# Performance work log

Hardware: AMD Instinct MI355X
Metric: run time of the kernel (lower is better)

## Reference

```python
import jax, jax.numpy as jnp
import numpy as np

N_NODES = 100000
N_EDGES = 3200000  # avg degree 32
D_IN = 128
D_OUT = 64
BN_EPS = 0.001


def setup_inputs() -> dict:
    key = jax.random.key(0)
    k1, k2, k3, k4, k5 = jax.random.split(key, 5)
    x = jax.random.normal(k1, (N_NODES, D_IN), dtype=jnp.float32)
    W = jax.random.normal(k2, (D_IN, D_OUT), dtype=jnp.float32) * 0.05
    edge_val = jax.random.uniform(k3, (N_EDGES,), dtype=jnp.float32)
    edge_src = jax.random.randint(k4, (N_EDGES,), 0, N_NODES, dtype=jnp.int32)
    edge_dst = jax.random.randint(k5, (N_EDGES,), 0, N_NODES, dtype=jnp.int32)
    return {"x": x, "W": W, "edge_val": edge_val,
            "edge_src": edge_src, "edge_dst": edge_dst}


def reference(x, W, edge_val, edge_src, edge_dst):
    # pre_sup = X @ W  (dense feature transform; dropout rate is 0 -> identity)
    pre_sup = x @ W  # [N, D_OUT]
    # support = A @ pre_sup, A given in COO form: A[dst, src] = edge_val
    msgs = edge_val[:, None] * pre_sup[edge_src]          # [E, D_OUT]
    out = jax.ops.segment_sum(msgs, edge_dst, num_segments=N_NODES)  # [N, D_OUT]
    # tf.nn.moments over all-but-last axis + batch_norm (no scale/offset, eps=1e-3)
    mean = jnp.mean(out, axis=0)
    var = jnp.var(out, axis=0)
    out = (out - mean) * jax.lax.rsqrt(var + BN_EPS)
    return jax.nn.relu(out)
```

## Files before the change

### kernel.cpp

```cpp
#include <hip/hip_runtime.h>
#include <stdint.h>

#define D_IN  128
#define D_OUT 64
#define BN_EPS 1e-3f

#define BIN_SHIFT 6
#define BIN_NODES 64
#define BIN_CAP   2560
#define CHUNK     8192
#define MAX_BINS  1600

typedef __attribute__((ext_vector_type(8))) short bf16x8;
typedef __attribute__((ext_vector_type(4))) float f32x4;

__device__ __forceinline__ ushort f32_to_bf16_rne(float f) {
  uint u = __float_as_uint(f);
  u += 0x7FFFu + ((u >> 16) & 1u);
  return (ushort)(u >> 16);
}
__device__ __forceinline__ float bf16_to_f32(ushort h) {
  return __uint_as_float((uint)h << 16);
}

__global__ __launch_bounds__(256) void gemm_mfma_kernel(
    const float* __restrict__ x, const float* __restrict__ W,
    ushort* __restrict__ pre16, int n_nodes, int n_tiles) {
  __shared__ ushort Wb[D_IN * D_OUT];
  const int t = threadIdx.x;
  for (int i = t; i < D_IN * D_OUT; i += 256) Wb[i] = f32_to_bf16_rne(W[i]);
  __syncthreads();

  const int lane = t & 63;
  const int wave = t >> 6;
  const int m = lane & 15;
  const int quad = lane >> 4;

  bf16x8 bfrag[4][4];
#pragma unroll
  for (int nt = 0; nt < 4; ++nt)
#pragma unroll
    for (int s = 0; s < 4; ++s)
#pragma unroll
      for (int j = 0; j < 8; ++j)
        bfrag[nt][s][j] =
            (short)Wb[(32 * s + quad * 8 + j) * D_OUT + nt * 16 + m];

  for (int tile = blockIdx.x; tile < n_tiles; tile += gridDim.x) {
    const int rbase = tile * 64 + wave * 16;
    const int row = rbase + m;
    const size_t rl = (size_t)min(row, n_nodes - 1);
    f32x4 acc0 = {0.f, 0.f, 0.f, 0.f}, acc1 = {0.f, 0.f, 0.f, 0.f};
    f32x4 acc2 = {0.f, 0.f, 0.f, 0.f}, acc3 = {0.f, 0.f, 0.f, 0.f};
#pragma unroll
    for (int s = 0; s < 4; ++s) {
      const float4 xa = *(const float4*)&x[rl * D_IN + s * 32 + quad * 8];
      const float4 xb = *(const float4*)&x[rl * D_IN + s * 32 + quad * 8 + 4];
      bf16x8 af;
      af[0] = (short)f32_to_bf16_rne(xa.x);
      af[1] = (short)f32_to_bf16_rne(xa.y);
      af[2] = (short)f32_to_bf16_rne(xa.z);
      af[3] = (short)f32_to_bf16_rne(xa.w);
      af[4] = (short)f32_to_bf16_rne(xb.x);
      af[5] = (short)f32_to_bf16_rne(xb.y);
      af[6] = (short)f32_to_bf16_rne(xb.z);
      af[7] = (short)f32_to_bf16_rne(xb.w);
      acc0 = __builtin_amdgcn_mfma_f32_16x16x32_bf16(af, bfrag[0][s], acc0, 0, 0, 0);
      acc1 = __builtin_amdgcn_mfma_f32_16x16x32_bf16(af, bfrag[1][s], acc1, 0, 0, 0);
      acc2 = __builtin_amdgcn_mfma_f32_16x16x32_bf16(af, bfrag[2][s], acc2, 0, 0, 0);
      acc3 = __builtin_amdgcn_mfma_f32_16x16x32_bf16(af, bfrag[3][s], acc3, 0, 0, 0);
    }
#pragma unroll
    for (int reg = 0; reg < 4; ++reg) {
      const int r = rbase + quad * 4 + reg;
      if (r < n_nodes) {
        ushort* po = &pre16[(size_t)r * D_OUT + m];
        po[0]  = f32_to_bf16_rne(acc0[reg]);
        po[16] = f32_to_bf16_rne(acc1[reg]);
        po[32] = f32_to_bf16_rne(acc2[reg]);
        po[48] = f32_to_bf16_rne(acc3[reg]);
      }
    }
  }
}

__global__ __launch_bounds__(256) void partition_kernel(
    const float* __restrict__ ev, const int* __restrict__ esrc,
    const int* __restrict__ edst, int* __restrict__ bin_cursor,
    uint2* __restrict__ bucket, int n_edges, int n_bins) {
  __shared__ int cnt[MAX_BINS];
  __shared__ int base[MAX_BINS];
  const int t = threadIdx.x;
  const int beg = blockIdx.x * CHUNK;
  const int end = min(beg + CHUNK, n_edges);

  for (int i = t; i < n_bins; i += 256) cnt[i] = 0;
  __syncthreads();

  for (int i = beg + t; i < end; i += 256)
    atomicAdd(&cnt[edst[i] >> BIN_SHIFT], 1);
  __syncthreads();

  for (int i = t; i < n_bins; i += 256) {
    const int c = cnt[i];
    int b = 0;
    if (c > 0) b = atomicAdd(&bin_cursor[i], c);
    if (b > BIN_CAP) b = BIN_CAP;
    base[i] = i * BIN_CAP + b;
    cnt[i] = 0;
  }
  __syncthreads();

  for (int i = beg + t; i < end; i += 256) {
    const int dst = edst[i];
    const int bin = dst >> BIN_SHIFT;
    const int r = atomicAdd(&cnt[bin], 1);
    const int pos = base[bin] + r;
    if (pos < (bin + 1) * BIN_CAP) {
      const uint w0 = ((uint)(dst & (BIN_NODES - 1)) << 17) | (uint)esrc[i];
      bucket[pos] = make_uint2(w0, __float_as_uint(ev[i]));
    }
  }
}

__global__ __launch_bounds__(256) void bin_sort_gather_kernel(
    const ushort* __restrict__ pre16, const uint2* __restrict__ bucket,
    const int* __restrict__ bin_cursor, float* __restrict__ out,
    float* __restrict__ stats, int n_nodes) {
  __shared__ uint s_src[BIN_CAP];
  __shared__ ushort s_val[BIN_CAP];
  __shared__ int s_hist[BIN_NODES];
  __shared__ int s_off[BIN_NODES + 1];
  __shared__ int s_cur[BIN_NODES];

  const int t = threadIdx.x;
  const int bin = blockIdx.x;
  const int cnt = min(bin_cursor[bin], BIN_CAP);
  const int64_t rbase = (int64_t)bin * BIN_CAP;

  if (t < BIN_NODES) s_hist[t] = 0;
  __syncthreads();

  for (int i = t; i < cnt; i += 256)
    atomicAdd(&s_hist[bucket[rbase + i].x >> 17], 1);
  __syncthreads();

  int own = (t < BIN_NODES) ? s_hist[t] : 0;
  for (int off = 1; off < BIN_NODES; off <<= 1) {
    int u = 0;
    if (t < BIN_NODES && t >= off) u = s_hist[t - off];
    __syncthreads();
    if (t < BIN_NODES) s_hist[t] += u;
    __syncthreads();
  }
  if (t < BIN_NODES) {
    const int e = s_hist[t] - own;
    s_off[t] = e;
    s_cur[t] = e;
  }
  if (t == 0) s_off[BIN_NODES] = cnt;
  __syncthreads();

  for (int i = t; i < cnt; i += 256) {
    const uint2 r = bucket[rbase + i];
    const int d = r.x >> 17;
    const int p = atomicAdd(&s_cur[d], 1);
    s_src[p] = r.x & 0x1FFFFu;
    s_val[p] = f32_to_bf16_rne(__uint_as_float(r.y));
  }
  __syncthreads();

  const int lane = t & 63;
  const int wave = t >> 6;
  const int half = lane >> 5;
  const int hl = lane & 31;
  const int node0 = bin * BIN_NODES;
  float csx = 0.f, csy = 0.f, cs2x = 0.f, cs2y = 0.f;

  for (int nl = wave; nl < BIN_NODES; nl += 4) {
    const int node = node0 + nl;
    if (node < n_nodes) {
      const int jb = s_off[nl], je = s_off[nl + 1];
      float a0x = 0.f, a0y = 0.f, a1x = 0.f, a1y = 0.f;
      int j = jb + half;
      for (; j + 2 < je; j += 4) {
        const uint src0 = s_src[j];
        const uint src1 = s_src[j + 2];
        const float v0 = bf16_to_f32(s_val[j]);
        const float v1 = bf16_to_f32(s_val[j + 2]);
        const uint p0 = *(const uint*)&pre16[(size_t)src0 * D_OUT + 2 * hl];
        const uint p1 = *(const uint*)&pre16[(size_t)src1 * D_OUT + 2 * hl];
        a0x += v0 * bf16_to_f32((ushort)(p0 & 0xFFFFu));
        a0y += v0 * bf16_to_f32((ushort)(p0 >> 16));
        a1x += v1 * bf16_to_f32((ushort)(p1 & 0xFFFFu));
        a1y += v1 * bf16_to_f32((ushort)(p1 >> 16));
      }
      if (j < je) {
        const uint src = s_src[j];
        const float v = bf16_to_f32(s_val[j]);
        const uint p = *(const uint*)&pre16[(size_t)src * D_OUT + 2 * hl];
        a0x += v * bf16_to_f32((ushort)(p & 0xFFFFu));
        a0y += v * bf16_to_f32((ushort)(p >> 16));
      }
      float ax = a0x + a1x, ay = a0y + a1y;
      ax += __shfl_xor(ax, 32);
      ay += __shfl_xor(ay, 32);
      if (half == 0) {
        *(float2*)&out[(size_t)node * D_OUT + 2 * hl] = make_float2(ax, ay);
        csx += ax;
        cs2x += ax * ax;
        csy += ay;
        cs2y += ay * ay;
      }
    }
  }
  __syncthreads();

  float* red = (float*)s_src;
  float* red2 = red + 256;
  if (half == 0) {
    red[wave * 64 + 2 * hl] = csx;
    red[wave * 64 + 2 * hl + 1] = csy;
    red2[wave * 64 + 2 * hl] = cs2x;
    red2[wave * 64 + 2 * hl + 1] = cs2y;
  }
  __syncthreads();
  if (t < 64) {
    float s = red[t] + red[64 + t] + red[128 + t] + red[192 + t];
    float s2 = red2[t] + red2[64 + t] + red2[128 + t] + red2[192 + t];
    atomicAdd(&stats[t], s);
    atomicAdd(&stats[64 + t], s2);
  }
}

__global__ __launch_bounds__(256) void norm_kernel(
    float* __restrict__ out, const float* __restrict__ stats, int64_t n_elems,
    float inv_n) {
  const int c = threadIdx.x & 63;
  const float mean = stats[c] * inv_n;
  const float var = stats[64 + c] * inv_n - mean * mean;
  const float scale = rsqrtf(var + BN_EPS);
  const int64_t stride = (int64_t)gridDim.x * 256;
  for (int64_t i = (int64_t)blockIdx.x * 256 + threadIdx.x; i < n_elems;
       i += stride) {
    const float v = (out[i] - mean) * scale;
    out[i] = v > 0.f ? v : 0.f;
  }
}

extern "C" void kernel_launch(void* const* d_in, const int* in_sizes, int n_in,
                              void* d_out, int out_size, void* d_ws,
                              size_t ws_size, hipStream_t stream) {
  const float* x = (const float*)d_in[0];
  const float* W = (const float*)d_in[1];
  const float* ev = (const float*)d_in[2];
  const int* esrc = (const int*)d_in[3];
  const int* edst = (const int*)d_in[4];

  const int n_nodes = in_sizes[0] / D_IN;
  const int n_edges = in_sizes[2];
  const int64_t n_out = (int64_t)n_nodes * D_OUT;
  const int n_bins = (n_nodes + BIN_NODES - 1) >> BIN_SHIFT;
  const int n_row_tiles = (n_nodes + 63) / 64;

  float* out = (float*)d_out;

  char* w = (char*)d_ws;
  ushort* pre16 = (ushort*)w;             w += (size_t)n_nodes * D_OUT * 2;
  int* bin_cursor = (int*)w;              w += (size_t)n_bins * 4;
  float* stats = (float*)w;               w += 128 * 4;
  w = (char*)(((uintptr_t)w + 7) & ~(uintptr_t)7);
  uint2* bucket = (uint2*)w;

  hipMemsetAsync(bin_cursor, 0, (size_t)n_bins * 4, stream);
  hipMemsetAsync(stats, 0, 128 * 4, stream);

  gemm_mfma_kernel<<<(n_row_tiles + 1) / 2, 256, 0, stream>>>(
      x, W, pre16, n_nodes, n_row_tiles);
  partition_kernel<<<(n_edges + CHUNK - 1) / CHUNK, 256, 0, stream>>>(
      ev, esrc, edst, bin_cursor, bucket, n_edges, n_bins);
  bin_sort_gather_kernel<<<n_bins, 256, 0, stream>>>(pre16, bucket, bin_cursor,
                                                     out, stats, n_nodes);
  norm_kernel<<<2048, 256, 0, stream>>>(out, stats, n_out,
                                        1.0f / (float)n_nodes);
}
```

Before: 346.3 us.

## Fuse GEMM and edge partition into one launch, halve bin size, stage buckets in LDS

The GEMM and edge-partition kernels become a single launch whose blocks branch on block index, with their shared memory overlaid through a union. The two independent phases can then run concurrently and one launch boundary disappears. Bins shrink from 64 to 32 nodes, so the gather kernel gets twice as many blocks. The gather kernel also reads each bin's bucket from global memory once into LDS instead of twice. The costs are more LDS per gather block, more bins for the partition blocks to count and reserve, and GEMM and partition blocks sharing one launch's resources.

Measured after the change: 402.7 us. 1.16x slower.

```diff
diff --git a/kernel.cpp b/kernel.cpp
--- a/kernel.cpp
+++ b/kernel.cpp
@@ -5,11 +5,11 @@
 #define D_OUT 64
 #define BN_EPS 1e-3f
 
-#define BIN_SHIFT 6
-#define BIN_NODES 64
-#define BIN_CAP   2560
+#define BIN_SHIFT 5
+#define BIN_NODES 32
+#define BIN_CAP   1280
 #define CHUNK     8192
-#define MAX_BINS  1600
+#define MAX_BINS  3328
 
 typedef __attribute__((ext_vector_type(8))) short bf16x8;
 typedef __attribute__((ext_vector_type(4))) float f32x4;
@@ -23,102 +23,109 @@
   return __uint_as_float((uint)h << 16);
 }
 
-__global__ __launch_bounds__(256) void gemm_mfma_kernel(
+struct PartLds {
+  int cnt[MAX_BINS];
+  int base[MAX_BINS];
+};
+union FusedLds {
+  ushort Wb[D_IN * D_OUT];
+  PartLds p;
+};
+
+__global__ __launch_bounds__(256) void gemm_part_kernel(
     const float* __restrict__ x, const float* __restrict__ W,
-    ushort* __restrict__ pre16, int n_nodes, int n_tiles) {
-  __shared__ ushort Wb[D_IN * D_OUT];
+    ushort* __restrict__ pre16, const float* __restrict__ ev,
+    const int* __restrict__ esrc, const int* __restrict__ edst,
+    int* __restrict__ bin_cursor, uint2* __restrict__ bucket, int n_nodes,
+    int n_tiles, int gemm_blocks, int n_edges, int n_bins) {
+  __shared__ FusedLds sh;
   const int t = threadIdx.x;
-  for (int i = t; i < D_IN * D_OUT; i += 256) Wb[i] = f32_to_bf16_rne(W[i]);
-  __syncthreads();
-
-  const int lane = t & 63;
-  const int wave = t >> 6;
-  const int m = lane & 15;
-  const int quad = lane >> 4;
-
-  bf16x8 bfrag[4][4];
-#pragma unroll
-  for (int nt = 0; nt < 4; ++nt)
-#pragma unroll
-    for (int s = 0; s < 4; ++s)
-#pragma unroll
-      for (int j = 0; j < 8; ++j)
-        bfrag[nt][s][j] =
-            (short)Wb[(32 * s + quad * 8 + j) * D_OUT + nt * 16 + m];
-
-  for (int tile = blockIdx.x; tile < n_tiles; tile += gridDim.x) {
-    const int rbase = tile * 64 + wave * 16;
-    const int row = rbase + m;
-    const size_t rl = (size_t)min(row, n_nodes - 1);
-    f32x4 acc0 = {0.f, 0.f, 0.f, 0.f}, acc1 = {0.f, 0.f, 0.f, 0.f};
-    f32x4 acc2 = {0.f, 0.f, 0.f, 0.f}, acc3 = {0.f, 0.f, 0.f, 0.f};
-#pragma unroll
-    for (int s = 0; s < 4; ++s) {
-      const float4 xa = *(const float4*)&x[rl * D_IN + s * 32 + quad * 8];
-      const float4 xb = *(const float4*)&x[rl * D_IN + s * 32 + quad * 8 + 4];
-      bf16x8 af;
-      af[0] = (short)f32_to_bf16_rne(xa.x);
-      af[1] = (short)f32_to_bf16_rne(xa.y);
-      af[2] = (short)f32_to_bf16_rne(xa.z);
-      af[3] = (short)f32_to_bf16_rne(xa.w);
-      af[4] = (short)f32_to_bf16_rne(xb.x);
-      af[5] = (short)f32_to_bf16_rne(xb.y);
-      af[6] = (short)f32_to_bf16_rne(xb.z);
-      af[7] = (short)f32_to_bf16_rne(xb.w);
-      acc0 = __builtin_amdgcn_mfma_f32_16x16x32_bf16(af, bfrag[0][s], acc0, 0, 0, 0);
-      acc1 = __builtin_amdgcn_mfma_f32_16x16x32_bf16(af, bfrag[1][s], acc1, 0, 0, 0);
-      acc2 = __builtin_amdgcn_mfma_f32_16x16x32_bf16(af, bfrag[2][s], acc2, 0, 0, 0);
-      acc3 = __builtin_amdgcn_mfma_f32_16x16x32_bf16(af, bfrag[3][s], acc3, 0, 0, 0);
-    }
-#pragma unroll
-    for (int reg = 0; reg < 4; ++reg) {
-      const int r = rbase + quad * 4 + reg;
-      if (r < n_nodes) {
-        ushort* po = &pre16[(size_t)r * D_OUT + m];
-        po[0]  = f32_to_bf16_rne(acc0[reg]);
-        po[16] = f32_to_bf16_rne(acc1[reg]);
-        po[32] = f32_to_bf16_rne(acc2[reg]);
-        po[48] = f32_to_bf16_rne(acc3[reg]);
-      }
-    }
-  }
-}
-
-__global__ __launch_bounds__(256) void partition_kernel(
-    const float* __restrict__ ev, const int* __restrict__ esrc,
-    const int* __restrict__ edst, int* __restrict__ bin_cursor,
-    uint2* __restrict__ bucket, int n_edges, int n_bins) {
-  __shared__ int cnt[MAX_BINS];
-  __shared__ int base[MAX_BINS];
-  const int t = threadIdx.x;
-  const int beg = blockIdx.x * CHUNK;
-  const int end = min(beg + CHUNK, n_edges);
-
-  for (int i = t; i < n_bins; i += 256) cnt[i] = 0;
-  __syncthreads();
-
-  for (int i = beg + t; i < end; i += 256)
-    atomicAdd(&cnt[edst[i] >> BIN_SHIFT], 1);
-  __syncthreads();
-
-  for (int i = t; i < n_bins; i += 256) {
-    const int c = cnt[i];
-    int b = 0;
-    if (c > 0) b = atomicAdd(&bin_cursor[i], c);
-    if (b > BIN_CAP) b = BIN_CAP;
-    base[i] = i * BIN_CAP + b;
-    cnt[i] = 0;
-  }
-  __syncthreads();
-
-  for (int i = beg + t; i < end; i += 256) {
-    const int dst = edst[i];
-    const int bin = dst >> BIN_SHIFT;
-    const int r = atomicAdd(&cnt[bin], 1);
-    const int pos = base[bin] + r;
-    if (pos < (bin + 1) * BIN_CAP) {
-      const uint w0 = ((uint)(dst & (BIN_NODES - 1)) << 17) | (uint)esrc[i];
-      bucket[pos] = make_uint2(w0, __float_as_uint(ev[i]));
+
+  if (blockIdx.x < gemm_blocks) {
+    for (int i = t; i < D_IN * D_OUT; i += 256) sh.Wb[i] = f32_to_bf16_rne(W[i]);
+    __syncthreads();
+
+    const int lane = t & 63;
+    const int wave = t >> 6;
+    const int m = lane & 15;
+    const int quad = lane >> 4;
+
+    bf16x8 bfrag[4][4];
+#pragma unroll
+    for (int nt = 0; nt < 4; ++nt)
+#pragma unroll
+      for (int s = 0; s < 4; ++s)
+#pragma unroll
+        for (int j = 0; j < 8; ++j)
+          bfrag[nt][s][j] =
+              (short)sh.Wb[(32 * s + quad * 8 + j) * D_OUT + nt * 16 + m];
+
+    for (int tile = blockIdx.x; tile < n_tiles; tile += gemm_blocks) {
+      const int rbase = tile * 64 + wave * 16;
+      const int row = rbase + m;
+      const size_t rl = (size_t)min(row, n_nodes - 1);
+      f32x4 acc0 = {0.f, 0.f, 0.f, 0.f}, acc1 = {0.f, 0.f, 0.f, 0.f};
+      f32x4 acc2 = {0.f, 0.f, 0.f, 0.f}, acc3 = {0.f, 0.f, 0.f, 0.f};
+#pragma unroll
+      for (int s = 0; s < 4; ++s) {
+        const float4 xa = *(const float4*)&x[rl * D_IN + s * 32 + quad * 8];
+        const float4 xb = *(const float4*)&x[rl * D_IN + s * 32 + quad * 8 + 4];
+        bf16x8 af;
+        af[0] = (short)f32_to_bf16_rne(xa.x);
+        af[1] = (short)f32_to_bf16_rne(xa.y);
+        af[2] = (short)f32_to_bf16_rne(xa.z);
+        af[3] = (short)f32_to_bf16_rne(xa.w);
+        af[4] = (short)f32_to_bf16_rne(xb.x);
+        af[5] = (short)f32_to_bf16_rne(xb.y);
+        af[6] = (short)f32_to_bf16_rne(xb.z);
+        af[7] = (short)f32_to_bf16_rne(xb.w);
+        acc0 = __builtin_amdgcn_mfma_f32_16x16x32_bf16(af, bfrag[0][s], acc0, 0, 0, 0);
+        acc1 = __builtin_amdgcn_mfma_f32_16x16x32_bf16(af, bfrag[1][s], acc1, 0, 0, 0);
+        acc2 = __builtin_amdgcn_mfma_f32_16x16x32_bf16(af, bfrag[2][s], acc2, 0, 0, 0);
+        acc3 = __builtin_amdgcn_mfma_f32_16x16x32_bf16(af, bfrag[3][s], acc3, 0, 0, 0);
+      }
+#pragma unroll
+      for (int reg = 0; reg < 4; ++reg) {
+        const int r = rbase + quad * 4 + reg;
+        if (r < n_nodes) {
+          ushort* po = &pre16[(size_t)r * D_OUT + m];
+          po[0]  = f32_to_bf16_rne(acc0[reg]);
+          po[16] = f32_to_bf16_rne(acc1[reg]);
+          po[32] = f32_to_bf16_rne(acc2[reg]);
+          po[48] = f32_to_bf16_rne(acc3[reg]);
+        }
+      }
+    }
+  } else {
+    const int beg = (blockIdx.x - gemm_blocks) * CHUNK;
+    const int end = min(beg + CHUNK, n_edges);
+
+    for (int i = t; i < n_bins; i += 256) sh.p.cnt[i] = 0;
+    __syncthreads();
+
+    for (int i = beg + t; i < end; i += 256)
+      atomicAdd(&sh.p.cnt[edst[i] >> BIN_SHIFT], 1);
+    __syncthreads();
+
+    for (int i = t; i < n_bins; i += 256) {
+      const int c = sh.p.cnt[i];
+      int b = 0;
+      if (c > 0) b = atomicAdd(&bin_cursor[i], c);
+      if (b > BIN_CAP) b = BIN_CAP;
+      sh.p.base[i] = i * BIN_CAP + b;
+      sh.p.cnt[i] = 0;
+    }
+    __syncthreads();
+
+    for (int i = beg + t; i < end; i += 256) {
+      const int dst = edst[i];
+      const int bin = dst >> BIN_SHIFT;
+      const int r = atomicAdd(&sh.p.cnt[bin], 1);
+      const int pos = sh.p.base[bin] + r;
+      if (pos < (bin + 1) * BIN_CAP) {
+        const uint w0 = ((uint)(dst & (BIN_NODES - 1)) << 17) | (uint)esrc[i];
+        bucket[pos] = make_uint2(w0, __float_as_uint(ev[i]));
+      }
     }
   }
 }
@@ -127,6 +134,7 @@
     const ushort* __restrict__ pre16, const uint2* __restrict__ bucket,
     const int* __restrict__ bin_cursor, float* __restrict__ out,
     float* __restrict__ stats, int n_nodes) {
+  __shared__ uint2 s_stage[BIN_CAP];
   __shared__ uint s_src[BIN_CAP];
   __shared__ ushort s_val[BIN_CAP];
   __shared__ int s_hist[BIN_NODES];
@@ -138,11 +146,12 @@
   const int cnt = min(bin_cursor[bin], BIN_CAP);
   const int64_t rbase = (int64_t)bin * BIN_CAP;
 
+  for (int i = t; i < cnt; i += 256) s_stage[i] = bucket[rbase + i];
   if (t < BIN_NODES) s_hist[t] = 0;
   __syncthreads();
 
   for (int i = t; i < cnt; i += 256)
-    atomicAdd(&s_hist[bucket[rbase + i].x >> 17], 1);
+    atomicAdd(&s_hist[s_stage[i].x >> 17], 1);
   __syncthreads();
 
   int own = (t < BIN_NODES) ? s_hist[t] : 0;
@@ -162,7 +171,7 @@
   __syncthreads();
 
   for (int i = t; i < cnt; i += 256) {
-    const uint2 r = bucket[rbase + i];
+    const uint2 r = s_stage[i];
     const int d = r.x >> 17;
     const int p = atomicAdd(&s_cur[d], 1);
     s_src[p] = r.x & 0x1FFFFu;
@@ -216,7 +225,7 @@
   }
   __syncthreads();
 
-  float* red = (float*)s_src;
+  float* red = (float*)s_stage;
   float* red2 = red + 256;
   if (half == 0) {
     red[wave * 64 + 2 * hl] = csx;
@@ -262,6 +271,8 @@
   const int64_t n_out = (int64_t)n_nodes * D_OUT;
   const int n_bins = (n_nodes + BIN_NODES - 1) >> BIN_SHIFT;
   const int n_row_tiles = (n_nodes + 63) / 64;
+  const int gemm_blocks = (n_row_tiles + 1) / 2;
+  const int part_blocks = (n_edges + CHUNK - 1) / CHUNK;
 
   float* out = (float*)d_out;
 
@@ -275,10 +286,9 @@
   hipMemsetAsync(bin_cursor, 0, (size_t)n_bins * 4, stream);
   hipMemsetAsync(stats, 0, 128 * 4, stream);
 
-  gemm_mfma_kernel<<<(n_row_tiles + 1) / 2, 256, 0, stream>>>(
-      x, W, pre16, n_nodes, n_row_tiles);
-  partition_kernel<<<(n_edges + CHUNK - 1) / CHUNK, 256, 0, stream>>>(
-      ev, esrc, edst, bin_cursor, bucket, n_edges, n_bins);
+  gemm_part_kernel<<<gemm_blocks + part_blocks, 256, 0, stream>>>(
+      x, W, pre16, ev, esrc, edst, bin_cursor, bucket, n_nodes, n_row_tiles,
+      gemm_blocks, n_edges, n_bins);
   bin_sort_gather_kernel<<<n_bins, 256, 0, stream>>>(pre16, bucket, bin_cursor,
                                                      out, stats, n_nodes);
   norm_kernel<<<2048, 256, 0, stream>>>(out, stats, n_out,
```
